# Optimization experiments

Hardware: AMD Instinct MI355X
Metric: run time of the kernel (lower is better)

## Reference

```python
import jax, jax.numpy as jnp
import numpy as np

N, E = 30000, 480000          # nodes, edges (avg degree 16)
DIM, DQK, H = 128, 128, 8     # dim_in = dim_v = 128, dim_qk = 128, heads
FD = DQK // H                 # kernel feature dim per head
DVH = DIM // H                # value dim per head


def setup_inputs() -> dict:
    key = jax.random.key(0)
    ks = jax.random.split(key, 12)
    g = lambda k, shape: jax.random.normal(k, shape, jnp.float32)
    return {
        "x": g(ks[0], (N, DIM)),
        "vec": g(ks[1], (N, 3, DIM)) * 0.1,
        "edge_vec": g(ks[2], (E, 3)),
        "edge_weight": jax.random.uniform(ks[3], (N, 1), jnp.float32),
        "W_fc1": g(ks[4], (DIM, 2 * DQK + DIM)) / np.sqrt(DIM),
        "W_fcv": g(ks[5], (DIM, 3 * DIM)) / np.sqrt(DIM),
        "b_fcv": jnp.zeros((3 * DIM,), jnp.float32),
        "W_fco": g(ks[6], (DIM, DIM)) / np.sqrt(DIM),
        "b_fco": jnp.zeros((DIM,), jnp.float32),
        "W_out": g(ks[7], (DIM, 3 * DIM)) / np.sqrt(DIM),
        "W_vecproj": g(ks[8], (DIM, 3 * DIM)) / np.sqrt(DIM),
        "W_equiv": g(ks[9], (DIM, DIM)) / np.sqrt(DIM),
        "ln_scale": jnp.ones((DIM,), jnp.float32),
        "ln_bias": jnp.zeros((DIM,), jnp.float32),
        "edge_index": jax.random.randint(ks[10], (2, E), 0, N),
    }


def _phi(z):
    # positive kernel feature map (elu + 1), per head: [N, DQK] -> [N, H, FD]
    return jax.nn.elu(z.reshape(z.shape[0], H, FD)) + 1.0


def reference(x, vec, edge_vec, edge_weight,
              W_fc1, W_fcv, b_fcv, W_fco, b_fco, W_out, W_vecproj, W_equiv,
              ln_scale, ln_bias, edge_index):
    # fc_1 -> q | k | non-attention residual
    h1 = x @ W_fc1
    q, k, non_att = h1[:, :DQK], h1[:, DQK:2 * DQK], h1[:, 2 * DQK:]
    # fc_v -> v | vec1 gate | vec2 gate
    pv = x @ W_fcv + b_fcv
    v, vec1, vec2 = pv[:, :DIM], pv[:, DIM:2 * DIM], pv[:, 2 * DIM:]

    # kernelized linear self-attention over the node set (order 1->1)
    qf, kf = _phi(q), _phi(k)                      # [N,H,FD]
    vh = v.reshape(N, H, DVH)                      # [N,H,DVH]
    kv = jnp.einsum('nhf,nhd->hfd', kf, vh)        # [H,FD,DVH]
    z = kf.sum(0)                                  # [H,FD]
    num = jnp.einsum('nhf,hfd->nhd', qf, kv)
    den = jnp.einsum('nhf,hf->nh', qf, z)[..., None] + 1e-6
    att = (num / den).reshape(N, DIM)

    # equivariant vector projections: v1p, v2p, v3p
    vp = jnp.einsum('nci,io->nco', vec, W_vecproj)  # [N,3,3*DIM]
    v1p, v2p, v3p = vp[..., :DIM], vp[..., DIM:2 * DIM], vp[..., 2 * DIM:]
    vec_dot = (v1p * v2p).sum(1)                    # [N,DIM]

    # MPNN propagate: per-edge vector messages, scatter-sum to destination
    src, dst = edge_index[0], edge_index[1]
    msg = vec[src] * vec1[src][:, None, :] + edge_vec[:, :, None] * vec2[src][:, None, :]
    vec_agg = jax.ops.segment_sum(msg, dst, num_segments=N)  # [N,3,DIM]

    # gated output combination (o1, o2, o3)
    o = att @ W_out
    o1, o2, o3 = o[:, :DIM], o[:, DIM:2 * DIM], o[:, 2 * DIM:]
    delta_x = vec_dot * o2 + o3
    delta_vec = v3p * o1[:, None, :] + vec_agg

    att_out = ((att + delta_x) @ W_fco + b_fco) * edge_weight
    out_x = non_att + att_out

    # LayerNorm over channel dim, then equivariant projection
    mu = delta_vec.mean(-1, keepdims=True)
    var = delta_vec.var(-1, keepdims=True)
    dvn = (delta_vec - mu) / jnp.sqrt(var + 1e-5) * ln_scale + ln_bias
    out_vec = dvn @ W_equiv
    return out_x, out_vec
```

## Files before the change

kernel.cpp:

```cpp
#include <hip/hip_runtime.h>
#include <math.h>

#define NN 30000
#define EE 480000
#define DIM 128
#define KVB 512

typedef __attribute__((ext_vector_type(8))) short bf16x8;
typedef __attribute__((ext_vector_type(8))) short s16x8;
typedef __attribute__((ext_vector_type(4))) short s16x4;
typedef __attribute__((ext_vector_type(4))) float f32x4;
typedef __attribute__((ext_vector_type(4))) float float4v;
typedef unsigned short ushort_t;

__device__ inline short f2bf(float f) {
    union { float f; unsigned u; } v; v.f = f;
    unsigned u = v.u;
    u += 0x7fffu + ((u >> 16) & 1u);
    return (short)(u >> 16);
}
__device__ inline float bf2f(unsigned short u) {
    union { unsigned u; float f; } v; v.u = ((unsigned)u) << 16; return v.f;
}
__device__ inline unsigned pack2(float a, float b) {
    return (unsigned)(ushort_t)f2bf(a) | ((unsigned)(ushort_t)f2bf(b) << 16);
}

__device__ inline bf16x8 cvt8(float4v lo, float4v hi) {
    bf16x8 r;
    r[0] = f2bf(lo[0]); r[1] = f2bf(lo[1]); r[2] = f2bf(lo[2]); r[3] = f2bf(lo[3]);
    r[4] = f2bf(hi[0]); r[5] = f2bf(hi[1]); r[6] = f2bf(hi[2]); r[7] = f2bf(hi[3]);
    return r;
}
__device__ inline void bf8_to_f(bf16x8 v, float4v& lo, float4v& hi) {
#pragma unroll
    for (int i = 0; i < 4; ++i) {
        lo[i] = bf2f((unsigned short)v[i]);
        hi[i] = bf2f((unsigned short)v[4 + i]);
    }
}

__global__ void pack_all(const float* __restrict__ fc1, const float* __restrict__ fcv,
                         const float* __restrict__ wout, const float* __restrict__ wvp,
                         const float* __restrict__ fco, const float* __restrict__ weq,
                         short* __restrict__ Wpk) {
    int fid = blockIdx.x * 4 + (threadIdx.x >> 6);
    int lane = threadIdx.x & 63;
    const float* src; int Nsrc, c0, f;
    if (fid < 96)       { src = fc1;  Nsrc = 384; c0 = 0;   f = fid; }
    else if (fid < 192) { src = fcv;  Nsrc = 384; c0 = 0;   f = fid - 96; }
    else if (fid < 288) { src = wout; Nsrc = 384; c0 = 0;   f = fid - 192; }
    else if (fid < 352) { src = wvp;  Nsrc = 384; c0 = 0;   f = fid - 288; }
    else if (fid < 384) { src = wvp;  Nsrc = 384; c0 = 256; f = fid - 352; }
    else if (fid < 416) { src = fco;  Nsrc = 128; c0 = 0;   f = fid - 384; }
    else                { src = weq;  Nsrc = 128; c0 = 0;   f = fid - 416; }
    int ct = f >> 2, kk = f & 3;
    int k0 = kk * 32 + (lane >> 4) * 8;
    int col = c0 + ct * 16 + (lane & 15);
    bf16x8 v;
#pragma unroll
    for (int i = 0; i < 8; ++i) v[i] = f2bf(src[(size_t)(k0 + i) * Nsrc + col]);
    *(bf16x8*)(Wpk + ((size_t)fid * 64 + lane) * 8) = v;
}

__global__ __launch_bounds__(256) void x_gemm(const float* __restrict__ in,
        const short* __restrict__ Wpk, const float* __restrict__ bfcv,
        ushort_t* __restrict__ h1, ushort_t* __restrict__ pv, int nrows) {
    const int lane = threadIdx.x & 63;
    const int wid = threadIdx.x >> 6;
    const int rbase = blockIdx.x * 128 + wid * 32;
    if (rbase >= nrows) return;
    const bool isPv = blockIdx.y >= 3;
    const int ct0 = (blockIdx.y - (isPv ? 3 : 0)) * 8;
    const short* W = Wpk + (isPv ? 96 * 512 : 0);
    ushort_t* out = isPv ? pv : h1;
    const int rlo = lane & 15, khi = (lane >> 4) * 8;
    bf16x8 a[2][4];
#pragma unroll
    for (int t = 0; t < 2; ++t) {
        int row = min(rbase + t * 16 + rlo, nrows - 1);
        const float* rp = in + (size_t)row * 128 + khi;
#pragma unroll
        for (int kk = 0; kk < 4; ++kk) {
            float4v lo = *(const float4v*)(rp + kk * 32);
            float4v hi = *(const float4v*)(rp + kk * 32 + 4);
            a[t][kk] = cvt8(lo, hi);
        }
    }
#pragma unroll
    for (int c = 0; c < 8; ++c) {
        const int ct = ct0 + c;
        bf16x8 b[4];
#pragma unroll
        for (int kk = 0; kk < 4; ++kk)
            b[kk] = *(const bf16x8*)(W + ((size_t)(ct * 4 + kk) * 64 + lane) * 8);
        f32x4 acc0 = {0.f, 0.f, 0.f, 0.f}, acc1 = {0.f, 0.f, 0.f, 0.f};
#pragma unroll
        for (int kk = 0; kk < 4; ++kk) {
            acc0 = __builtin_amdgcn_mfma_f32_16x16x32_bf16(a[0][kk], b[kk], acc0, 0, 0, 0);
            acc1 = __builtin_amdgcn_mfma_f32_16x16x32_bf16(a[1][kk], b[kk], acc1, 0, 0, 0);
        }
        const int col = ct * 16 + rlo;
        const float bv = isPv ? bfcv[col] : 0.f;
#pragma unroll
        for (int r = 0; r < 4; ++r) {
            int row0 = rbase + (lane >> 4) * 4 + r;
            int row1 = row0 + 16;
            if (row0 < nrows) out[(size_t)row0 * 384 + col] = (ushort_t)f2bf(acc0[r] + bv);
            if (row1 < nrows) out[(size_t)row1 * 384 + col] = (ushort_t)f2bf(acc1[r] + bv);
        }
    }
}

template<int COLS, int CT_PER, bool BIAS, typename InT, typename OutT>
__global__ __launch_bounds__(256) void mfma_gemm(const InT* __restrict__ in,
        const short* __restrict__ Wpk, const float* __restrict__ bias,
        OutT* __restrict__ out, int nrows) {
    const int lane = threadIdx.x & 63;
    const int wid = threadIdx.x >> 6;
    const int rbase = blockIdx.x * 128 + wid * 32;
    if (rbase >= nrows) return;
    const int ct0 = blockIdx.y * CT_PER;
    const int rlo = lane & 15, khi = (lane >> 4) * 8;
    bf16x8 a[2][4];
#pragma unroll
    for (int t = 0; t < 2; ++t) {
        int row = min(rbase + t * 16 + rlo, nrows - 1);
        const InT* rp = in + (size_t)row * 128 + khi;
#pragma unroll
        for (int kk = 0; kk < 4; ++kk) {
            if constexpr (sizeof(InT) == 4) {
                float4v lo = *(const float4v*)(rp + kk * 32);
                float4v hi = *(const float4v*)(rp + kk * 32 + 4);
                a[t][kk] = cvt8(lo, hi);
            } else {
                a[t][kk] = *(const bf16x8*)(rp + kk * 32);
            }
        }
    }
#pragma unroll
    for (int c = 0; c < CT_PER; ++c) {
        const int ct = ct0 + c;
        bf16x8 b[4];
#pragma unroll
        for (int kk = 0; kk < 4; ++kk)
            b[kk] = *(const bf16x8*)(Wpk + ((size_t)(ct * 4 + kk) * 64 + lane) * 8);
        f32x4 acc0 = {0.f, 0.f, 0.f, 0.f}, acc1 = {0.f, 0.f, 0.f, 0.f};
#pragma unroll
        for (int kk = 0; kk < 4; ++kk) {
            acc0 = __builtin_amdgcn_mfma_f32_16x16x32_bf16(a[0][kk], b[kk], acc0, 0, 0, 0);
            acc1 = __builtin_amdgcn_mfma_f32_16x16x32_bf16(a[1][kk], b[kk], acc1, 0, 0, 0);
        }
        const int col = ct * 16 + rlo;
        const float bv = BIAS ? bias[col] : 0.f;
#pragma unroll
        for (int r = 0; r < 4; ++r) {
            int row0 = rbase + (lane >> 4) * 4 + r;
            int row1 = row0 + 16;
            if constexpr (sizeof(OutT) == 4) {
                if (row0 < nrows) out[(size_t)row0 * COLS + col] = acc0[r] + bv;
                if (row1 < nrows) out[(size_t)row1 * COLS + col] = acc1[r] + bv;
            } else {
                if (row0 < nrows) out[(size_t)row0 * COLS + col] = (OutT)f2bf(acc0[r] + bv);
                if (row1 < nrows) out[(size_t)row1 * COLS + col] = (OutT)f2bf(acc1[r] + bv);
            }
        }
    }
}

__global__ __launch_bounds__(256) void vp_gemm(const float* __restrict__ in,
        const short* __restrict__ Wpk, ushort_t* __restrict__ vp12,
        ushort_t* __restrict__ v3p, int nrows) {
    const int lane = threadIdx.x & 63;
    const int wid = threadIdx.x >> 6;
    const int rbase = blockIdx.x * 128 + wid * 32;
    if (rbase >= nrows) return;
    const int rlo = lane & 15, khi = (lane >> 4) * 8;
    bf16x8 a[2][4];
#pragma unroll
    for (int t = 0; t < 2; ++t) {
        int row = min(rbase + t * 16 + rlo, nrows - 1);
        const float* rp = in + (size_t)row * 128 + khi;
#pragma unroll
        for (int kk = 0; kk < 4; ++kk) {
            float4v lo = *(const float4v*)(rp + kk * 32);
            float4v hi = *(const float4v*)(rp + kk * 32 + 4);
            a[t][kk] = cvt8(lo, hi);
        }
    }
    for (int ct = 0; ct < 24; ++ct) {
        bf16x8 b[4];
#pragma unroll
        for (int kk = 0; kk < 4; ++kk)
            b[kk] = *(const bf16x8*)(Wpk + ((size_t)(ct * 4 + kk) * 64 + lane) * 8);
        f32x4 acc0 = {0.f, 0.f, 0.f, 0.f}, acc1 = {0.f, 0.f, 0.f, 0.f};
#pragma unroll
        for (int kk = 0; kk < 4; ++kk) {
            acc0 = __builtin_amdgcn_mfma_f32_16x16x32_bf16(a[0][kk], b[kk], acc0, 0, 0, 0);
            acc1 = __builtin_amdgcn_mfma_f32_16x16x32_bf16(a[1][kk], b[kk], acc1, 0, 0, 0);
        }
        const int col = ct * 16 + rlo;
#pragma unroll
        for (int r = 0; r < 4; ++r) {
            int row0 = rbase + (lane >> 4) * 4 + r;
            int row1 = row0 + 16;
            if (col < 256) {
                if (row0 < nrows) vp12[(size_t)row0 * 256 + col] = (ushort_t)f2bf(acc0[r]);
                if (row1 < nrows) vp12[(size_t)row1 * 256 + col] = (ushort_t)f2bf(acc1[r]);
            } else {
                if (row0 < nrows) v3p[(size_t)row0 * 128 + col - 256] = (ushort_t)f2bf(acc0[r]);
                if (row1 < nrows) v3p[(size_t)row1 * 128 + col - 256] = (ushort_t)f2bf(acc1[r]);
            }
        }
    }
}

__global__ __launch_bounds__(256) void kv_part(const ushort_t* __restrict__ h1,
        const ushort_t* __restrict__ pv, float* __restrict__ slab) {
    __shared__ float kf_s[8][DIM];
    __shared__ float v_s[8][DIM];
    const int tid = threadIdx.x;
    const int rpb = (NN + KVB - 1) / KVB;
    const int n0 = blockIdx.x * rpb;
    const int n1 = min(n0 + rpb, NN);
    const int base = tid * 8;
    const int hf = base >> 4;
    const int h = hf >> 4;
    const int d0 = base & 15;
    const int lr = tid >> 5;
    const int lg = tid & 31;
    const bool isK = lg < 16;
    const int le = (lg & 15) * 8;
    float acc[8];
#pragma unroll
    for (int i = 0; i < 8; ++i) acc[i] = 0.f;
    float zacc = 0.f;
    s16x8 praw = {0,0,0,0,0,0,0,0};
    bool pvalid = false;
    {
        int n = n0 + lr;
        pvalid = n < n1;
        if (pvalid) {
            const ushort_t* src = isK ? (h1 + (size_t)n * 384 + 128 + le)
                                      : (pv + (size_t)n * 384 + le);
            praw = *(const s16x8*)src;
        }
    }
    for (int nt = n0; nt < n1; nt += 8) {
        __syncthreads();
        float v8[8];
#pragma unroll
        for (int i = 0; i < 8; ++i) v8[i] = pvalid ? bf2f((unsigned short)praw[i]) : 0.f;
        if (pvalid && isK) {
#pragma unroll
            for (int i = 0; i < 8; ++i) v8[i] = v8[i] > 0.f ? v8[i] + 1.f : expf(v8[i]);
        }
        float* dst = (isK ? kf_s[lr] : v_s[lr]) + le;
#pragma unroll
        for (int i = 0; i < 8; ++i) dst[i] = v8[i];
        __syncthreads();
        {
            int n = nt + 8 + lr;
            pvalid = n < n1;
            if (pvalid) {
                const ushort_t* src = isK ? (h1 + (size_t)n * 384 + 128 + le)
                                          : (pv + (size_t)n * 384 + le);
                praw = *(const s16x8*)src;
            }
        }
#pragma unroll
        for (int r = 0; r < 8; ++r) {
            float kfv = kf_s[r][hf];
#pragma unroll
            for (int i = 0; i < 8; ++i) acc[i] = fmaf(kfv, v_s[r][h * 16 + d0 + i], acc[i]);
            if (tid < 128) zacc += kf_s[r][tid];
        }
    }
    float* row = slab + (size_t)blockIdx.x * 2176;
#pragma unroll
    for (int i = 0; i < 8; ++i) row[base + i] = acc[i];
    if (tid < 128) row[2048 + tid] = zacc;
}

__global__ void kv_final(const float* __restrict__ slab, float* __restrict__ kvz) {
    int i = blockIdx.x * 256 + threadIdx.x;
    if (i >= 2176) return;
    float a[8];
#pragma unroll
    for (int j = 0; j < 8; ++j) a[j] = 0.f;
    for (int b = 0; b < KVB; b += 8) {
#pragma unroll
        for (int j = 0; j < 8; ++j) a[j] += slab[(size_t)(b + j) * 2176 + i];
    }
    kvz[i] = ((a[0] + a[1]) + (a[2] + a[3])) + ((a[4] + a[5]) + (a[6] + a[7]));
}

__global__ void attn_apply(const ushort_t* __restrict__ h1, const float* __restrict__ kvz,
                           ushort_t* __restrict__ att) {
    __shared__ float kv_s[8 * 16 * 17];
    __shared__ float z_s[DIM];
    __shared__ float qf_s[8][DIM];
    const int tid = threadIdx.x;
    const int n0 = blockIdx.x * 8;
    for (int i = tid; i < 2048; i += 128) {
        int hf = i >> 4, d = i & 15;
        kv_s[hf * 17 + d] = kvz[i];
    }
    z_s[tid] = kvz[2048 + tid];
#pragma unroll
    for (int r = 0; r < 8; ++r) {
        float qv = bf2f(h1[(size_t)(n0 + r) * 384 + tid]);
        qf_s[r][tid] = qv > 0.f ? qv + 1.f : expf(qv);
    }
    __syncthreads();
    const int h = tid >> 4, d = tid & 15;
#pragma unroll
    for (int r = 0; r < 8; ++r) {
        float num = 0.f, den = 0.f;
#pragma unroll
        for (int f = 0; f < 16; ++f) {
            float q = qf_s[r][h * 16 + f];
            num = fmaf(q, kv_s[(h * 16 + f) * 17 + d], num);
            den = fmaf(q, z_s[h * 16 + f], den);
        }
        att[(size_t)(n0 + r) * DIM + tid] = (ushort_t)f2bf(num / (den + 1e-6f));
    }
}

__global__ __launch_bounds__(256) void vecdot_reduce(const ushort_t* __restrict__ vp12,
        const float* __restrict__ vec, const ushort_t* __restrict__ pv,
        ushort_t* __restrict__ vdot, ushort_t* __restrict__ P) {
    const int tid = threadIdx.x;
    const int c2 = tid & 63;
    const int sub = tid >> 6;
    const int n0 = blockIdx.x * 8;
#pragma unroll
    for (int rr = 0; rr < 2; ++rr) {
        const int n = n0 + sub + rr * 4;
        float a0 = 0.f, a1 = 0.f;
#pragma unroll
        for (int c = 0; c < 3; ++c) {
            unsigned u1 = *(const unsigned*)(vp12 + (size_t)(3 * n + c) * 256 + 2 * c2);
            unsigned u2 = *(const unsigned*)(vp12 + (size_t)(3 * n + c) * 256 + 128 + 2 * c2);
            a0 = fmaf(bf2f((unsigned short)u1), bf2f((unsigned short)u2), a0);
            a1 = fmaf(bf2f((unsigned short)(u1 >> 16)), bf2f((unsigned short)(u2 >> 16)), a1);
        }
        *(unsigned*)(vdot + (size_t)n * 128 + 2 * c2) = pack2(a0, a1);
        unsigned uv1 = *(const unsigned*)(pv + (size_t)n * 384 + 128 + 2 * c2);
        unsigned uv2 = *(const unsigned*)(pv + (size_t)n * 384 + 256 + 2 * c2);
        float v1x = bf2f((unsigned short)uv1), v1y = bf2f((unsigned short)(uv1 >> 16));
        s16x8 pk;
        pk[0] = (short)(ushort_t)(uv2 & 0xffffu);
        pk[4] = (short)(ushort_t)(uv2 >> 16);
#pragma unroll
        for (int c = 0; c < 3; ++c) {
            float2 vc = *(const float2*)(vec + ((size_t)n * 3 + c) * 128 + 2 * c2);
            pk[1 + c] = f2bf(vc.x * v1x);
            pk[5 + c] = f2bf(vc.y * v1y);
        }
        *(s16x8*)(P + (size_t)n * 512 + (size_t)c2 * 8) = pk;
    }
}

__global__ void hist_kernel(const int* __restrict__ eidx, int* __restrict__ cnt) {
    int e = blockIdx.x * 256 + threadIdx.x;
    if (e < EE) atomicAdd(&cnt[eidx[EE + e]], 1);
}

__global__ void scan_kernel(const int* __restrict__ cnt, int* __restrict__ off,
                            int* __restrict__ pos) {
    __shared__ int wsum[16];
    const int tid = threadIdx.x;
    const int lane = tid & 63, wv = tid >> 6;
    const int PER = 30;
    const int base = tid * PER;
    int local[PER];
    int s = 0;
#pragma unroll
    for (int i = 0; i < PER; ++i) {
        int idx = base + i;
        int c = (idx < NN) ? cnt[idx] : 0;
        local[i] = s;
        s += c;
    }
    int incl = s;
#pragma unroll
    for (int d = 1; d < 64; d <<= 1) {
        int v = __shfl_up(incl, d, 64);
        if (lane >= d) incl += v;
    }
    if (lane == 63) wsum[wv] = incl;
    __syncthreads();
    if (wv == 0 && lane < 16) {
        int v = wsum[lane];
        int iv = v;
#pragma unroll
        for (int d = 1; d < 16; d <<= 1) {
            int u = __shfl_up(iv, d, 16);
            if (lane >= d) iv += u;
        }
        wsum[lane] = iv - v;
    }
    __syncthreads();
    const int carry = wsum[wv] + (incl - s);
#pragma unroll
    for (int i = 0; i < PER; ++i) {
        int idx = base + i;
        if (idx < NN) {
            int v = carry + local[i];
            off[idx] = v;
            pos[idx] = v;
        }
    }
    if (tid == 1023) off[NN] = wsum[15] + incl;
}

__global__ void scatter_kernel(const int* __restrict__ eidx, const float* __restrict__ evec,
                               int* __restrict__ pos, int4* __restrict__ sorted4) {
    int e = blockIdx.x * 256 + threadIdx.x;
    if (e >= EE) return;
    int dst = eidx[EE + e];
    int src = eidx[e];
    float e0 = evec[(size_t)e * 3 + 0];
    float e1 = evec[(size_t)e * 3 + 1];
    float e2 = evec[(size_t)e * 3 + 2];
    int p = atomicAdd(&pos[dst], 1);
    sorted4[p] = make_int4(src, __float_as_int(e0), __float_as_int(e1), __float_as_int(e2));
}

__global__ __launch_bounds__(256) void edge_agg_kernel(
        const int* __restrict__ off, const int4* __restrict__ sorted4,
        const ushort_t* __restrict__ P, ushort_t* __restrict__ agg) {
    __shared__ int srcs[128];
    __shared__ float evs[3][128];
    __shared__ float part[3][128];
    const int dst = blockIdx.x;
    const int tid = threadIdx.x;
    const int g = tid >> 7, o = tid & 127;
    const int j0 = off[dst], j1 = off[dst + 1];
    float a0 = 0.f, a1 = 0.f, a2 = 0.f;
    for (int jt = j0; jt < j1; jt += 128) {
        const int m = min(128, j1 - jt);
        if (tid < m) {
            int4 w = sorted4[jt + tid];
            srcs[tid] = w.x;
            evs[0][tid] = __int_as_float(w.y);
            evs[1][tid] = __int_as_float(w.z);
            evs[2][tid] = __int_as_float(w.w);
        }
        __syncthreads();
        int jj = g;
        for (; jj + 14 < m; jj += 16) {
            s16x4 pk[8];
#pragma unroll
            for (int u = 0; u < 8; ++u)
                pk[u] = *(const s16x4*)(P + (size_t)srcs[jj + 2 * u] * 512 + o * 4);
#pragma unroll
            for (int u = 0; u < 8; ++u) {
                int e = jj + 2 * u;
                float v2 = bf2f((unsigned short)pk[u][0]);
                a0 += fmaf(evs[0][e], v2, bf2f((unsigned short)pk[u][1]));
                a1 += fmaf(evs[1][e], v2, bf2f((unsigned short)pk[u][2]));
                a2 += fmaf(evs[2][e], v2, bf2f((unsigned short)pk[u][3]));
            }
        }
        for (; jj < m; jj += 2) {
            s16x4 pk = *(const s16x4*)(P + (size_t)srcs[jj] * 512 + o * 4);
            float v2 = bf2f((unsigned short)pk[0]);
            a0 += fmaf(evs[0][jj], v2, bf2f((unsigned short)pk[1]));
            a1 += fmaf(evs[1][jj], v2, bf2f((unsigned short)pk[2]));
            a2 += fmaf(evs[2][jj], v2, bf2f((unsigned short)pk[3]));
        }
        __syncthreads();
    }
    if (g == 1) { part[0][o] = a0; part[1][o] = a1; part[2][o] = a2; }
    __syncthreads();
    if (g == 0) {
        a0 += part[0][o]; a1 += part[1][o]; a2 += part[2][o];
        agg[((size_t)dst * 3 + 0) * DIM + o] = (ushort_t)f2bf(a0);
        agg[((size_t)dst * 3 + 1) * DIM + o] = (ushort_t)f2bf(a1);
        agg[((size_t)dst * 3 + 2) * DIM + o] = (ushort_t)f2bf(a2);
    }
}

__global__ __launch_bounds__(256) void outx_mfma(const ushort_t* __restrict__ att,
        const ushort_t* __restrict__ vdot, const ushort_t* __restrict__ o,
        const short* __restrict__ Wpk, const float* __restrict__ bfco,
        const ushort_t* __restrict__ h1, const float* __restrict__ ew,
        float* __restrict__ outx) {
    const int lane = threadIdx.x & 63;
    const int wid = threadIdx.x >> 6;
    const int rbase = blockIdx.x * 128 + wid * 32;
    if (rbase >= NN) return;
    const int ct0 = blockIdx.y * 4;
    const int rlo = lane & 15, khi = (lane >> 4) * 8;
    bf16x8 a[2][4];
#pragma unroll
    for (int t = 0; t < 2; ++t) {
        int row = min(rbase + t * 16 + rlo, NN - 1);
        const ushort_t* pa = att + (size_t)row * 128 + khi;
        const ushort_t* pd = vdot + (size_t)row * 128 + khi;
        const ushort_t* po = o + (size_t)row * 384 + khi;
#pragma unroll
        for (int kk = 0; kk < 4; ++kk) {
            int kb = kk * 32;
            float4v al, ah, dl, dh, o2l, o2h, o3l, o3h;
            bf8_to_f(*(const bf16x8*)(pa + kb), al, ah);
            bf8_to_f(*(const bf16x8*)(pd + kb), dl, dh);
            bf8_to_f(*(const bf16x8*)(po + 128 + kb), o2l, o2h);
            bf8_to_f(*(const bf16x8*)(po + 256 + kb), o3l, o3h);
            a[t][kk] = cvt8(al + dl * o2l + o3l, ah + dh * o2h + o3h);
        }
    }
    float ewv[2][4];
#pragma unroll
    for (int t = 0; t < 2; ++t)
#pragma unroll
        for (int r = 0; r < 4; ++r)
            ewv[t][r] = ew[min(rbase + t * 16 + (lane >> 4) * 4 + r, NN - 1)];
#pragma unroll
    for (int c = 0; c < 4; ++c) {
        const int ct = ct0 + c;
        bf16x8 b[4];
#pragma unroll
        for (int kk = 0; kk < 4; ++kk)
            b[kk] = *(const bf16x8*)(Wpk + ((size_t)(ct * 4 + kk) * 64 + lane) * 8);
        f32x4 acc0 = {0.f, 0.f, 0.f, 0.f}, acc1 = {0.f, 0.f, 0.f, 0.f};
#pragma unroll
        for (int kk = 0; kk < 4; ++kk) {
            acc0 = __builtin_amdgcn_mfma_f32_16x16x32_bf16(a[0][kk], b[kk], acc0, 0, 0, 0);
            acc1 = __builtin_amdgcn_mfma_f32_16x16x32_bf16(a[1][kk], b[kk], acc1, 0, 0, 0);
        }
        const int col = ct * 16 + rlo;
        const float bv = bfco[col];
#pragma unroll
        for (int r = 0; r < 4; ++r) {
            int row0 = rbase + (lane >> 4) * 4 + r;
            if (row0 < NN)
                outx[(size_t)row0 * 128 + col] =
                    bf2f(h1[(size_t)row0 * 384 + 256 + col]) + (acc0[r] + bv) * ewv[0][r];
            int row1 = row0 + 16;
            if (row1 < NN)
                outx[(size_t)row1 * 128 + col] =
                    bf2f(h1[(size_t)row1 * 384 + 256 + col]) + (acc1[r] + bv) * ewv[1][r];
        }
    }
}

__global__ __launch_bounds__(256) void outvec_ln(const ushort_t* __restrict__ v3p,
        const ushort_t* __restrict__ o, const ushort_t* __restrict__ agg,
        const float* __restrict__ ln_scale, const float* __restrict__ ln_bias,
        ushort_t* __restrict__ dvn) {
    const int tid = threadIdx.x;
    const int c2 = tid & 63;
    const int row = blockIdx.x * 4 + (tid >> 6);
    const int n = row / 3;
    unsigned uv3 = *(const unsigned*)(v3p + (size_t)row * 128 + 2 * c2);
    unsigned uo1 = *(const unsigned*)(o + (size_t)n * 384 + 2 * c2);
    unsigned uag = *(const unsigned*)(agg + (size_t)row * 128 + 2 * c2);
    float dv0 = fmaf(bf2f((unsigned short)uv3), bf2f((unsigned short)uo1),
                     bf2f((unsigned short)uag));
    float dv1 = fmaf(bf2f((unsigned short)(uv3 >> 16)), bf2f((unsigned short)(uo1 >> 16)),
                     bf2f((unsigned short)(uag >> 16)));
    float s = dv0 + dv1;
    float s2 = fmaf(dv0, dv0, dv1 * dv1);
#pragma unroll
    for (int d = 1; d < 64; d <<= 1) {
        s += __shfl_xor(s, d, 64);
        s2 += __shfl_xor(s2, d, 64);
    }
    float mu = s * (1.f / 128.f);
    float rstd = rsqrtf(s2 * (1.f / 128.f) - mu * mu + 1e-5f);
    float r0 = fmaf((dv0 - mu) * rstd, ln_scale[2 * c2], ln_bias[2 * c2]);
    float r1 = fmaf((dv1 - mu) * rstd, ln_scale[2 * c2 + 1], ln_bias[2 * c2 + 1]);
    *(unsigned*)(dvn + (size_t)row * 128 + 2 * c2) = pack2(r0, r1);
}

extern "C" void kernel_launch(void* const* d_in, const int* in_sizes, int n_in,
                              void* d_out, int out_size, void* d_ws, size_t ws_size,
                              hipStream_t stream) {
    const float* x          = (const float*)d_in[0];
    const float* vec        = (const float*)d_in[1];
    const float* edge_vec   = (const float*)d_in[2];
    const float* edge_weight= (const float*)d_in[3];
    const float* W_fc1      = (const float*)d_in[4];
    const float* W_fcv      = (const float*)d_in[5];
    const float* b_fcv      = (const float*)d_in[6];
    const float* W_fco      = (const float*)d_in[7];
    const float* b_fco      = (const float*)d_in[8];
    const float* W_out      = (const float*)d_in[9];
    const float* W_vecproj  = (const float*)d_in[10];
    const float* W_equiv    = (const float*)d_in[11];
    const float* ln_scale   = (const float*)d_in[12];
    const float* ln_bias    = (const float*)d_in[13];
    const int*   edge_index = (const int*)d_in[14];

    float* out_x   = (float*)d_out;
    float* out_vec = out_x + (size_t)NN * DIM;
    ushort_t* Pb = (ushort_t*)d_out;

    float* ws   = (float*)d_ws;
    ushort_t* h1_b   = (ushort_t*)ws;
    ushort_t* pv_b   = h1_b + 11520000;
    ushort_t* att_b  = pv_b + 11520000;
    ushort_t* vdot_b = att_b + 3840000;
    ushort_t* o_b    = vdot_b + 3840000;
    ushort_t* agg_b  = o_b + 11520000;
    ushort_t* v3p_b  = agg_b + 11520000;
    float* kvz  = (float*)(v3p_b + 11520000);
    ushort_t* vp12_b = o_b;
    float* slab = (float*)o_b;
    ushort_t* dvn_b = pv_b;
    int* cnt    = (int*)(kvz + 2176);
    int* off    = cnt + NN;
    int* pos    = off + NN + 1;
    size_t soff = ((size_t)(pos + NN - (int*)ws) + 3) & ~(size_t)3;
    int4* sorted4 = (int4*)((int*)ws + soff);
    short* Wpk  = (short*)((int*)ws + soff + (size_t)4 * EE);
    short* pk_fc1  = Wpk;
    short* pk_wout = Wpk + 192 * 512;
    short* pk_vp   = Wpk + 288 * 512;
    short* pk_fco  = Wpk + 384 * 512;
    short* pk_weq  = Wpk + 416 * 512;

    hipMemsetAsync(cnt, 0, NN * sizeof(int), stream);

    pack_all<<<112, 256, 0, stream>>>(W_fc1, W_fcv, W_out, W_vecproj, W_fco, W_equiv, Wpk);

    hist_kernel<<<(EE + 255) / 256, 256, 0, stream>>>(edge_index, cnt);
    scan_kernel<<<1, 1024, 0, stream>>>(cnt, off, pos);
    scatter_kernel<<<(EE + 255) / 256, 256, 0, stream>>>(edge_index, edge_vec, pos, sorted4);

    const int gN = (NN + 127) / 128;
    const int g3N = (3 * NN + 127) / 128;
    x_gemm<<<dim3(gN, 6), 256, 0, stream>>>(x, pk_fc1, b_fcv, h1_b, pv_b, NN);
    kv_part<<<KVB, 256, 0, stream>>>(h1_b, pv_b, slab);
    kv_final<<<9, 256, 0, stream>>>(slab, kvz);
    attn_apply<<<NN / 8, 128, 0, stream>>>(h1_b, kvz, att_b);
    vp_gemm<<<g3N, 256, 0, stream>>>(vec, pk_vp, vp12_b, v3p_b, 3 * NN);
    vecdot_reduce<<<NN / 8, 256, 0, stream>>>(vp12_b, vec, pv_b, vdot_b, Pb);
    mfma_gemm<384, 8, false, ushort_t, ushort_t><<<dim3(gN, 3), 256, 0, stream>>>(att_b, pk_wout, nullptr, o_b, NN);
    edge_agg_kernel<<<NN, 256, 0, stream>>>(off, sorted4, Pb, agg_b);
    outx_mfma<<<dim3(gN, 2), 256, 0, stream>>>(att_b, vdot_b, o_b, pk_fco, b_fco, h1_b, edge_weight, out_x);
    outvec_ln<<<(3 * NN) / 4, 256, 0, stream>>>(v3p_b, o_b, agg_b, ln_scale, ln_bias, dvn_b);
    mfma_gemm<128, 8, false, ushort_t, float><<<g3N, 256, 0, stream>>>(dvn_b, pk_weq, nullptr, out_vec, 3 * NN);
}
```

Baseline: 399.4 us.

## Fuse LayerNorm into W_equiv GEMM, share x loads across fc1/fcv, simplify edge loop

The LayerNorm over delta_vec now runs inside the W_equiv MFMA GEMM. Each wave normalizes its A-tile rows in registers, so the bf16 dvn intermediate is no longer written and re-read and one kernel launch goes away. x_gemm now computes both the h1 and pv output halves in one block, which halves the number of times x is loaded and converted to bf16, but each block does twice the work with half as many blocks. The edge aggregation loop drops its scalar tail and uses clamped loads with a predicate instead. This adds redundant loads for partial groups and raises register pressure in the fused kernel.

```diff
diff --git a/kernel.cpp b/kernel.cpp
--- a/kernel.cpp
+++ b/kernel.cpp
@@ -70,10 +70,7 @@
     const int wid = threadIdx.x >> 6;
     const int rbase = blockIdx.x * 128 + wid * 32;
     if (rbase >= nrows) return;
-    const bool isPv = blockIdx.y >= 3;
-    const int ct0 = (blockIdx.y - (isPv ? 3 : 0)) * 8;
-    const short* W = Wpk + (isPv ? 96 * 512 : 0);
-    ushort_t* out = isPv ? pv : h1;
+    const int ct0 = blockIdx.y * 8;
     const int rlo = lane & 15, khi = (lane >> 4) * 8;
     bf16x8 a[2][4];
 #pragma unroll
@@ -88,26 +85,31 @@
         }
     }
 #pragma unroll
-    for (int c = 0; c < 8; ++c) {
-        const int ct = ct0 + c;
-        bf16x8 b[4];
-#pragma unroll
-        for (int kk = 0; kk < 4; ++kk)
-            b[kk] = *(const bf16x8*)(W + ((size_t)(ct * 4 + kk) * 64 + lane) * 8);
-        f32x4 acc0 = {0.f, 0.f, 0.f, 0.f}, acc1 = {0.f, 0.f, 0.f, 0.f};
-#pragma unroll
-        for (int kk = 0; kk < 4; ++kk) {
-            acc0 = __builtin_amdgcn_mfma_f32_16x16x32_bf16(a[0][kk], b[kk], acc0, 0, 0, 0);
-            acc1 = __builtin_amdgcn_mfma_f32_16x16x32_bf16(a[1][kk], b[kk], acc1, 0, 0, 0);
-        }
-        const int col = ct * 16 + rlo;
-        const float bv = isPv ? bfcv[col] : 0.f;
-#pragma unroll
-        for (int r = 0; r < 4; ++r) {
-            int row0 = rbase + (lane >> 4) * 4 + r;
-            int row1 = row0 + 16;
-            if (row0 < nrows) out[(size_t)row0 * 384 + col] = (ushort_t)f2bf(acc0[r] + bv);
-            if (row1 < nrows) out[(size_t)row1 * 384 + col] = (ushort_t)f2bf(acc1[r] + bv);
+    for (int half = 0; half < 2; ++half) {
+        const short* W = Wpk + half * 96 * 512;
+        ushort_t* out = half ? pv : h1;
+#pragma unroll
+        for (int c = 0; c < 8; ++c) {
+            const int ct = ct0 + c;
+            bf16x8 b[4];
+#pragma unroll
+            for (int kk = 0; kk < 4; ++kk)
+                b[kk] = *(const bf16x8*)(W + ((size_t)(ct * 4 + kk) * 64 + lane) * 8);
+            f32x4 acc0 = {0.f, 0.f, 0.f, 0.f}, acc1 = {0.f, 0.f, 0.f, 0.f};
+#pragma unroll
+            for (int kk = 0; kk < 4; ++kk) {
+                acc0 = __builtin_amdgcn_mfma_f32_16x16x32_bf16(a[0][kk], b[kk], acc0, 0, 0, 0);
+                acc1 = __builtin_amdgcn_mfma_f32_16x16x32_bf16(a[1][kk], b[kk], acc1, 0, 0, 0);
+            }
+            const int col = ct * 16 + rlo;
+            const float bv = half ? bfcv[col] : 0.f;
+#pragma unroll
+            for (int r = 0; r < 4; ++r) {
+                int row0 = rbase + (lane >> 4) * 4 + r;
+                int row1 = row0 + 16;
+                if (row0 < nrows) out[(size_t)row0 * 384 + col] = (ushort_t)f2bf(acc0[r] + bv);
+                if (row1 < nrows) out[(size_t)row1 * 384 + col] = (ushort_t)f2bf(acc1[r] + bv);
+            }
         }
     }
 }
@@ -449,27 +451,23 @@
             evs[2][tid] = __int_as_float(w.w);
         }
         __syncthreads();
-        int jj = g;
-        for (; jj + 14 < m; jj += 16) {
+        for (int jj = g; jj < m; jj += 16) {
             s16x4 pk[8];
 #pragma unroll
-            for (int u = 0; u < 8; ++u)
-                pk[u] = *(const s16x4*)(P + (size_t)srcs[jj + 2 * u] * 512 + o * 4);
+            for (int u = 0; u < 8; ++u) {
+                int e = min(jj + 2 * u, m - 1);
+                pk[u] = *(const s16x4*)(P + (size_t)srcs[e] * 512 + o * 4);
+            }
 #pragma unroll
             for (int u = 0; u < 8; ++u) {
                 int e = jj + 2 * u;
-                float v2 = bf2f((unsigned short)pk[u][0]);
-                a0 += fmaf(evs[0][e], v2, bf2f((unsigned short)pk[u][1]));
-                a1 += fmaf(evs[1][e], v2, bf2f((unsigned short)pk[u][2]));
-                a2 += fmaf(evs[2][e], v2, bf2f((unsigned short)pk[u][3]));
-            }
-        }
-        for (; jj < m; jj += 2) {
-            s16x4 pk = *(const s16x4*)(P + (size_t)srcs[jj] * 512 + o * 4);
-            float v2 = bf2f((unsigned short)pk[0]);
-            a0 += fmaf(evs[0][jj], v2, bf2f((unsigned short)pk[1]));
-            a1 += fmaf(evs[1][jj], v2, bf2f((unsigned short)pk[2]));
-            a2 += fmaf(evs[2][jj], v2, bf2f((unsigned short)pk[3]));
+                if (e < m) {
+                    float v2 = bf2f((unsigned short)pk[u][0]);
+                    a0 += fmaf(evs[0][e], v2, bf2f((unsigned short)pk[u][1]));
+                    a1 += fmaf(evs[1][e], v2, bf2f((unsigned short)pk[u][2]));
+                    a2 += fmaf(evs[2][e], v2, bf2f((unsigned short)pk[u][3]));
+                }
+            }
         }
         __syncthreads();
     }
@@ -547,33 +545,78 @@
     }
 }
 
-__global__ __launch_bounds__(256) void outvec_ln(const ushort_t* __restrict__ v3p,
+__global__ __launch_bounds__(256) void outvec_fused(const ushort_t* __restrict__ v3p,
         const ushort_t* __restrict__ o, const ushort_t* __restrict__ agg,
         const float* __restrict__ ln_scale, const float* __restrict__ ln_bias,
-        ushort_t* __restrict__ dvn) {
-    const int tid = threadIdx.x;
-    const int c2 = tid & 63;
-    const int row = blockIdx.x * 4 + (tid >> 6);
-    const int n = row / 3;
-    unsigned uv3 = *(const unsigned*)(v3p + (size_t)row * 128 + 2 * c2);
-    unsigned uo1 = *(const unsigned*)(o + (size_t)n * 384 + 2 * c2);
-    unsigned uag = *(const unsigned*)(agg + (size_t)row * 128 + 2 * c2);
-    float dv0 = fmaf(bf2f((unsigned short)uv3), bf2f((unsigned short)uo1),
-                     bf2f((unsigned short)uag));
-    float dv1 = fmaf(bf2f((unsigned short)(uv3 >> 16)), bf2f((unsigned short)(uo1 >> 16)),
-                     bf2f((unsigned short)(uag >> 16)));
-    float s = dv0 + dv1;
-    float s2 = fmaf(dv0, dv0, dv1 * dv1);
-#pragma unroll
-    for (int d = 1; d < 64; d <<= 1) {
-        s += __shfl_xor(s, d, 64);
-        s2 += __shfl_xor(s2, d, 64);
-    }
-    float mu = s * (1.f / 128.f);
-    float rstd = rsqrtf(s2 * (1.f / 128.f) - mu * mu + 1e-5f);
-    float r0 = fmaf((dv0 - mu) * rstd, ln_scale[2 * c2], ln_bias[2 * c2]);
-    float r1 = fmaf((dv1 - mu) * rstd, ln_scale[2 * c2 + 1], ln_bias[2 * c2 + 1]);
-    *(unsigned*)(dvn + (size_t)row * 128 + 2 * c2) = pack2(r0, r1);
+        const short* __restrict__ Wpk, float* __restrict__ outv, int nrows) {
+    const int lane = threadIdx.x & 63;
+    const int wid = threadIdx.x >> 6;
+    const int rbase = blockIdx.x * 128 + wid * 32;
+    if (rbase >= nrows) return;
+    const int rlo = lane & 15, khi = (lane >> 4) * 8;
+    float ls[4][8], lb[4][8];
+#pragma unroll
+    for (int kk = 0; kk < 4; ++kk)
+#pragma unroll
+        for (int i = 0; i < 8; ++i) {
+            ls[kk][i] = ln_scale[khi + kk * 32 + i];
+            lb[kk][i] = ln_bias[khi + kk * 32 + i];
+        }
+    bf16x8 a[2][4];
+#pragma unroll
+    for (int t = 0; t < 2; ++t) {
+        int row = min(rbase + t * 16 + rlo, nrows - 1);
+        int n = row / 3;
+        float dv[4][8];
+        float s = 0.f, s2 = 0.f;
+#pragma unroll
+        for (int kk = 0; kk < 4; ++kk) {
+            bf16x8 v3 = *(const bf16x8*)(v3p + (size_t)row * 128 + khi + kk * 32);
+            bf16x8 oo = *(const bf16x8*)(o + (size_t)n * 384 + khi + kk * 32);
+            bf16x8 ag = *(const bf16x8*)(agg + (size_t)row * 128 + khi + kk * 32);
+#pragma unroll
+            for (int i = 0; i < 8; ++i) {
+                float v = fmaf(bf2f((unsigned short)v3[i]), bf2f((unsigned short)oo[i]),
+                               bf2f((unsigned short)ag[i]));
+                dv[kk][i] = v;
+                s += v;
+                s2 = fmaf(v, v, s2);
+            }
+        }
+        s += __shfl_xor(s, 16, 64);  s2 += __shfl_xor(s2, 16, 64);
+        s += __shfl_xor(s, 32, 64);  s2 += __shfl_xor(s2, 32, 64);
+        float mu = s * (1.f / 128.f);
+        float rstd = rsqrtf(s2 * (1.f / 128.f) - mu * mu + 1e-5f);
+#pragma unroll
+        for (int kk = 0; kk < 4; ++kk) {
+            bf16x8 r;
+#pragma unroll
+            for (int i = 0; i < 8; ++i)
+                r[i] = f2bf(fmaf((dv[kk][i] - mu) * rstd, ls[kk][i], lb[kk][i]));
+            a[t][kk] = r;
+        }
+    }
+#pragma unroll
+    for (int ct = 0; ct < 8; ++ct) {
+        bf16x8 b[4];
+#pragma unroll
+        for (int kk = 0; kk < 4; ++kk)
+            b[kk] = *(const bf16x8*)(Wpk + ((size_t)(ct * 4 + kk) * 64 + lane) * 8);
+        f32x4 acc0 = {0.f, 0.f, 0.f, 0.f}, acc1 = {0.f, 0.f, 0.f, 0.f};
+#pragma unroll
+        for (int kk = 0; kk < 4; ++kk) {
+            acc0 = __builtin_amdgcn_mfma_f32_16x16x32_bf16(a[0][kk], b[kk], acc0, 0, 0, 0);
+            acc1 = __builtin_amdgcn_mfma_f32_16x16x32_bf16(a[1][kk], b[kk], acc1, 0, 0, 0);
+        }
+        const int col = ct * 16 + rlo;
+#pragma unroll
+        for (int r = 0; r < 4; ++r) {
+            int row0 = rbase + (lane >> 4) * 4 + r;
+            int row1 = row0 + 16;
+            if (row0 < nrows) outv[(size_t)row0 * 128 + col] = acc0[r];
+            if (row1 < nrows) outv[(size_t)row1 * 128 + col] = acc1[r];
+        }
+    }
 }
 
 extern "C" void kernel_launch(void* const* d_in, const int* in_sizes, int n_in,
@@ -610,7 +653,6 @@
     float* kvz  = (float*)(v3p_b + 11520000);
     ushort_t* vp12_b = o_b;
     float* slab = (float*)o_b;
-    ushort_t* dvn_b = pv_b;
     int* cnt    = (int*)(kvz + 2176);
     int* off    = cnt + NN;
     int* pos    = off + NN + 1;
@@ -633,7 +675,7 @@
 
     const int gN = (NN + 127) / 128;
     const int g3N = (3 * NN + 127) / 128;
-    x_gemm<<<dim3(gN, 6), 256, 0, stream>>>(x, pk_fc1, b_fcv, h1_b, pv_b, NN);
+    x_gemm<<<dim3(gN, 3), 256, 0, stream>>>(x, pk_fc1, b_fcv, h1_b, pv_b, NN);
     kv_part<<<KVB, 256, 0, stream>>>(h1_b, pv_b, slab);
     kv_final<<<9, 256, 0, stream>>>(slab, kvz);
     attn_apply<<<NN / 8, 128, 0, stream>>>(h1_b, kvz, att_b);
@@ -642,6 +684,6 @@
     mfma_gemm<384, 8, false, ushort_t, ushort_t><<<dim3(gN, 3), 256, 0, stream>>>(att_b, pk_wout, nullptr, o_b, NN);
     edge_agg_kernel<<<NN, 256, 0, stream>>>(off, sorted4, Pb, agg_b);
     outx_mfma<<<dim3(gN, 2), 256, 0, stream>>>(att_b, vdot_b, o_b, pk_fco, b_fco, h1_b, edge_weight, out_x);
-    outvec_ln<<<(3 * NN) / 4, 256, 0, stream>>>(v3p_b, o_b, agg_b, ln_scale, ln_bias, dvn_b);
-    mfma_gemm<128, 8, false, ushort_t, float><<<g3N, 256, 0, stream>>>(dvn_b, pk_weq, nullptr, out_vec, 3 * NN);
-}
+    outvec_fused<<<g3N, 256, 0, stream>>>(v3p_b, o_b, agg_b, ln_scale, ln_bias, pk_weq,
+                                          out_vec, 3 * NN);
+}
```

Result: faster. 369.6 us (median of 2 runs) (-7.5%).
